# Optimization experiments

Measured on AMD Instinct MI355X. Metric: run time of the kernel, lower is better.

## Reference

```python
import jax, jax.numpy as jnp
import numpy as np

N, E, F_IN, HID, HEADS, B, CLASSES = 50000, 800000, 128, 64, 4, 512, 2


def setup_inputs() -> dict:
    key = jax.random.key(0)
    ks = jax.random.split(key, 20)
    s = 0.05
    inp = {
        "x": jax.random.normal(ks[0], (N, F_IN), jnp.float32),
        "edge_index": jax.random.randint(ks[1], (2, E), 0, N, jnp.int32),
        "batch": jnp.sort(jax.random.randint(ks[2], (N,), 0, B, jnp.int32)),
        # GCN layers (3): layer0 F_IN->HID, layers 1,2 HID->HID
        "gcn_w0": jax.random.normal(ks[3], (F_IN, HID), jnp.float32) * s,
        "gcn_b0": jnp.zeros((HID,), jnp.float32),
        "gcn_w1": jax.random.normal(ks[4], (HID, HID), jnp.float32) * s,
        "gcn_b1": jnp.zeros((HID,), jnp.float32),
        "gcn_w2": jax.random.normal(ks[5], (HID, HID), jnp.float32) * s,
        "gcn_b2": jnp.zeros((HID,), jnp.float32),
        # GAT: W [HID, HEADS*HID], attention vectors [HEADS, HID], bias [HID] (concat=False)
        "gat_w": jax.random.normal(ks[6], (HID, HEADS * HID), jnp.float32) * s,
        "gat_att_src": jax.random.normal(ks[7], (HEADS, HID), jnp.float32) * s,
        "gat_att_dst": jax.random.normal(ks[8], (HEADS, HID), jnp.float32) * s,
        "gat_b": jnp.zeros((HID,), jnp.float32),
        # MLP head
        "lin1_w": jax.random.normal(ks[9], (HID, HID // 2), jnp.float32) * s,
        "lin1_b": jnp.zeros((HID // 2,), jnp.float32),
        "lin2_w": jax.random.normal(ks[10], (HID // 2, CLASSES), jnp.float32) * s,
        "lin2_b": jnp.zeros((CLASSES,), jnp.float32),
    }
    return inp


def _forward(x, edge_index, batch,
             gcn_w0, gcn_b0, gcn_w1, gcn_b1, gcn_w2, gcn_b2,
             gat_w, gat_att_src, gat_att_dst, gat_b,
             lin1_w, lin1_b, lin2_w, lin2_b):
    n = x.shape[0]
    loop = jnp.arange(n, dtype=edge_index.dtype)
    src = jnp.concatenate([edge_index[0], loop])  # [E+N] with self-loops
    dst = jnp.concatenate([edge_index[1], loop])

    # symmetric GCN normalization (self-loops included, deg >= 1)
    deg = jax.ops.segment_sum(jnp.ones_like(dst, dtype=x.dtype), dst, num_segments=n)
    dinv = jax.lax.rsqrt(jnp.maximum(deg, 1.0))
    norm = dinv[src] * dinv[dst]  # [E+N]

    for W, b in ((gcn_w0, gcn_b0), (gcn_w1, gcn_b1), (gcn_w2, gcn_b2)):
        h = x @ W  # [N, HID]
        x = jax.ops.segment_sum(h[src] * norm[:, None], dst, num_segments=n) + b
        x = jax.nn.relu(x)  # dropout is identity in eval mode

    # GAT layer (heads=HEADS, concat=False -> mean over heads)
    H, C = gat_att_src.shape
    h = (x @ gat_w).reshape(n, H, C)  # [N, H, C]
    a_src = jnp.einsum('nhc,hc->nh', h, gat_att_src)
    a_dst = jnp.einsum('nhc,hc->nh', h, gat_att_dst)
    e = jax.nn.leaky_relu(a_src[src] + a_dst[dst], 0.2)  # [E+N, H]
    m = jax.ops.segment_max(e, dst, num_segments=n)      # per-dst softmax max
    p = jnp.exp(e - m[dst])
    denom = jax.ops.segment_sum(p, dst, num_segments=n)
    alpha = p / denom[dst]                                # [E+N, H]
    out = jax.ops.segment_sum(h[src] * alpha[:, :, None], dst, num_segments=n)
    x = jax.nn.relu(out.mean(axis=1) + gat_b)             # [N, HID]

    # global mean pool + global max pool over graphs
    cnt = jax.ops.segment_sum(jnp.ones((n,), x.dtype), batch, num_segments=B)
    mean_p = jax.ops.segment_sum(x, batch, num_segments=B) / jnp.maximum(cnt, 1.0)[:, None]
    max_p = jax.ops.segment_max(x, batch, num_segments=B)
    max_p = jnp.where(cnt[:, None] > 0, max_p, 0.0)
    g = mean_p + max_p  # [B, HID]

    g = jax.nn.relu(g @ lin1_w + lin1_b)
    return g @ lin2_w + lin2_b  # [B, CLASSES]


def reference(x, edge_index, batch,
              gcn_w0, gcn_b0, gcn_w1, gcn_b1, gcn_w2, gcn_b2,
              gat_w, gat_att_src, gat_att_dst, gat_b,
              lin1_w, lin1_b, lin2_w, lin2_b):
    return _forward(x, edge_index, batch,
                    gcn_w0, gcn_b0, gcn_w1, gcn_b1, gcn_w2, gcn_b2,
                    gat_w, gat_att_src, gat_att_dst, gat_b,
                    lin1_w, lin1_b, lin2_w, lin2_b)
```

## Files before the change

kernel.cpp:

```cpp
#include <hip/hip_runtime.h>
#include <math.h>

typedef short bf8 __attribute__((ext_vector_type(8)));
typedef _Float16 h8 __attribute__((ext_vector_type(8)));
typedef float f4 __attribute__((ext_vector_type(4)));
typedef unsigned short ushort_t;

#define BRANGE 128
#define NB_E 256

__device__ __forceinline__ int ilanebcast(int v, int l) {
  return __builtin_amdgcn_readlane(v, l);
}

__device__ __forceinline__ float wave_sum(float v) {
#pragma unroll
  for (int off = 32; off > 0; off >>= 1) v += __shfl_xor(v, off, 64);
  return v;
}

__device__ __forceinline__ ushort_t f2bf(float x) {
  unsigned int u = __float_as_uint(x);
  return (ushort_t)((u + 0x7fffu + ((u >> 16) & 1u)) >> 16);
}
__device__ __forceinline__ float b2f(ushort_t h) {
  return __uint_as_float(((unsigned int)h) << 16);
}

__global__ __launch_bounds__(256) void k_ehist(const int* __restrict__ dst,
                                               int* __restrict__ bhistT, int E, int nbuk) {
  __shared__ int h[512];
  int b = blockIdx.x, tid = threadIdx.x;
  for (int i = tid; i < nbuk; i += 256) h[i] = 0;
  __syncthreads();
  int chunk = (E + gridDim.x - 1) / gridDim.x;
  int e0 = b * chunk, e1 = min(E, e0 + chunk);
  for (int e = e0 + tid; e < e1; e += 256) atomicAdd(&h[dst[e] >> 7], 1);
  __syncthreads();
  for (int i = tid; i < nbuk; i += 256) bhistT[i * NB_E + b] = h[i];
}

__global__ __launch_bounds__(256) void k_btot(const int* __restrict__ bhistT,
                                              int* __restrict__ bcnt, int nb) {
  __shared__ int sm[256];
  int b = blockIdx.x, tid = threadIdx.x;
  sm[tid] = (tid < nb) ? bhistT[b * NB_E + tid] : 0;
  __syncthreads();
  for (int off = 128; off > 0; off >>= 1) {
    if (tid < off) sm[tid] += sm[tid + off];
    __syncthreads();
  }
  if (tid == 0) bcnt[b] = sm[0];
}

__global__ __launch_bounds__(512) void k_bscan(
    const int* __restrict__ bcnt, int* __restrict__ edgebase, int nbuk,
    int* __restrict__ rowstart, int n, int E) {
  __shared__ int smem[512];
  int t = threadIdx.x;
  int v = (t < nbuk) ? bcnt[t] : 0;
  smem[t] = v;
  __syncthreads();
  for (int off = 1; off < 512; off <<= 1) {
    int u = (t >= off) ? smem[t - off] : 0;
    __syncthreads();
    smem[t] += u;
    __syncthreads();
  }
  if (t < nbuk) edgebase[t] = smem[t] - v;
  if (t == 0) rowstart[n] = E + n;
}

__global__ __launch_bounds__(256) void k_bbase(int* __restrict__ bhistT,
                                               const int* __restrict__ edgebase,
                                               int nb) {
  __shared__ int sm[256];
  int b = blockIdx.x, tid = threadIdx.x;
  int v = (tid < nb) ? bhistT[b * NB_E + tid] : 0;
  sm[tid] = v;
  __syncthreads();
  for (int off = 1; off < 256; off <<= 1) {
    int u = (tid >= off) ? sm[tid - off] : 0;
    __syncthreads();
    sm[tid] += u;
    __syncthreads();
  }
  if (tid < nb) bhistT[b * NB_E + tid] = edgebase[b] + sm[tid] - v;
}

__global__ __launch_bounds__(256) void k_ebucket(
    const int* __restrict__ es, const int* __restrict__ ed,
    const int* __restrict__ bhistT, int* __restrict__ bedges, int E, int nbuk) {
  __shared__ int cur[512];
  int b = blockIdx.x, tid = threadIdx.x;
  for (int i = tid; i < nbuk; i += 256) cur[i] = bhistT[i * NB_E + b];
  __syncthreads();
  int chunk = (E + gridDim.x - 1) / gridDim.x;
  int e0 = b * chunk, e1 = min(E, e0 + chunk);
  for (int e = e0 + tid; e < e1; e += 256) {
    int s = es[e], d = ed[e];
    int pos = atomicAdd(&cur[d >> 7], 1);
    bedges[pos] = (s << 7) | (d & 127);
  }
}

__global__ __launch_bounds__(256) void k_ebsort(
    const int* __restrict__ bedges, const int* __restrict__ edgebase,
    const int* __restrict__ bcnt, int* __restrict__ colidx,
    int* __restrict__ rowstart, float* __restrict__ dinv, int n) {
  __shared__ int h[128];
  __shared__ int c[128];
  int b = blockIdx.x, tid = threadIdx.x;
  int nodes0 = b * BRANGE;
  int nnode = min(BRANGE, n - nodes0);
  int ebase = edgebase[b], ecnt = bcnt[b];
  int colbase = ebase + nodes0;
  if (tid < 128) h[tid] = (tid < nnode) ? 1 : 0;
  __syncthreads();
  for (int k = ebase + tid; k < ebase + ecnt; k += 256)
    atomicAdd(&h[bedges[k] & 127], 1);
  __syncthreads();
  int own = (tid < 128) ? h[tid] : 0;
  for (int off = 1; off < 128; off <<= 1) {
    int t = (tid >= off && tid < 128) ? h[tid - off] : 0;
    __syncthreads();
    if (tid < 128) h[tid] += t;
    __syncthreads();
  }
  if (tid < nnode) {
    int excl = h[tid] - own;
    int node = nodes0 + tid;
    rowstart[node] = colbase + excl;
    dinv[node] = 1.0f / sqrtf((float)own);
    colidx[colbase + excl] = node;
    c[tid] = excl + 1;
  }
  __syncthreads();
  for (int k = ebase + tid; k < ebase + ecnt; k += 256) {
    int p = bedges[k];
    int pos = atomicAdd(&c[p & 127], 1);
    colidx[colbase + pos] = p >> 7;
  }
}


__global__ void k_wswz0(const float* __restrict__ W, ushort_t* __restrict__ Bh,
                        ushort_t* __restrict__ Bl) {
  int e = blockIdx.x * 256 + threadIdx.x;
  if (e >= 4 * 4 * 64) return;
  int lane = e & 63, kc = (e >> 6) & 3, ct = e >> 8;
  int k0 = kc * 32 + (lane >> 4) * 8;
  int col = ct * 16 + (lane & 15);
#pragma unroll
  for (int j = 0; j < 8; j++) {
    float w = W[(k0 + j) * 64 + col];
    ushort_t h = f2bf(w);
    Bh[(size_t)e * 8 + j] = h;
    Bl[(size_t)e * 8 + j] = f2bf(w - b2f(h));
  }
}

__global__ void k_wswz1(const float* __restrict__ W, _Float16* __restrict__ Bh,
                        _Float16* __restrict__ Bl) {
  int e = blockIdx.x * 256 + threadIdx.x;
  if (e >= 8 * 64) return;
  int lane = e & 63, kc = (e >> 6) & 1, ct = e >> 7;
  int k0 = kc * 32 + (lane >> 4) * 8;
  int col = ct * 16 + (lane & 15);
#pragma unroll
  for (int j = 0; j < 8; j++) {
    float w = W[(k0 + j) * 64 + col];
    _Float16 h = (_Float16)w;
    Bh[(size_t)e * 8 + j] = h;
    Bl[(size_t)e * 8 + j] = (_Float16)(w - (float)h);
  }
}

__global__ void k_wswzg(const float* __restrict__ W, _Float16* __restrict__ Bh,
                        _Float16* __restrict__ Bl) {
  int e = blockIdx.x * 256 + threadIdx.x;
  if (e >= 4 * 8 * 64) return;
  int lane = e & 63, kc = (e >> 6) & 7, ct = e >> 9;
  int k0 = kc * 32 + (lane >> 4) * 8;
  int col = ct * 16 + (lane & 15);
#pragma unroll
  for (int j = 0; j < 8; j++) {
    int k = k0 + j;
    float w = W[(k & 63) * 256 + (k >> 6) * 64 + col];
    _Float16 h = (_Float16)w;
    Bh[(size_t)e * 8 + j] = h;
    Bl[(size_t)e * 8 + j] = (_Float16)(w - (float)h);
  }
}

__global__ void k_qpre(const float* __restrict__ W, const float* __restrict__ att_s,
                       const float* __restrict__ att_d,
                       float* __restrict__ q_src, float* __restrict__ q_dst) {
  int t = threadIdx.x;
  int h = t >> 6, k = t & 63;
  float ss = 0.0f, sd = 0.0f;
  for (int c = 0; c < 64; c++) {
    float w = W[k * 256 + h * 64 + c];
    ss = fmaf(w, att_s[h * 64 + c], ss);
    sd = fmaf(w, att_d[h * 64 + c], sd);
  }
  q_src[h * 64 + k] = ss;
  q_dst[h * 64 + k] = sd;
}

__global__ void k_qswz(const float* __restrict__ q_src, const float* __restrict__ q_dst,
                       _Float16* __restrict__ Bq) {
  int e = threadIdx.x;
  if (e >= 128) return;
  int lane = e & 63, kc = e >> 6;
  int k0 = kc * 32 + (lane >> 4) * 8;
  int col = lane & 15;
#pragma unroll
  for (int j = 0; j < 8; j++) {
    int k = k0 + j;
    float v = (col < 4) ? q_src[col * 64 + k]
                        : ((col < 8) ? q_dst[(col - 4) * 64 + k] : 0.0f);
    Bq[(size_t)e * 8 + j] = (_Float16)v;
  }
}

__global__ __launch_bounds__(256) void k_gemm0_mfma(
    const float* __restrict__ X, const ushort_t* __restrict__ Bh,
    const ushort_t* __restrict__ Bl, const float* __restrict__ dinv,
    _Float16* __restrict__ H, int n, int ntiles) {
  int tid = threadIdx.x, lane = tid & 63, wave = tid >> 6;
  int m = lane & 15, q = lane >> 4;
  for (int tile = blockIdx.x * 4 + wave; tile < ntiles; tile += gridDim.x * 4) {
    int ra = tile * 16 + m;
    if (ra >= n) ra = n - 1;
    const float* xrow = X + (size_t)ra * 128;
    f4 acc[4];
#pragma unroll
    for (int ct = 0; ct < 4; ct++) acc[ct] = (f4){0.f, 0.f, 0.f, 0.f};
#pragma unroll 2
    for (int kc = 0; kc < 4; kc++) {
      int ko = kc * 32 + q * 8;
      float4 xa = *(const float4*)(xrow + ko);
      float4 xb = *(const float4*)(xrow + ko + 4);
      float f[8] = {xa.x, xa.y, xa.z, xa.w, xb.x, xb.y, xb.z, xb.w};
      union { ushort_t u[8]; bf8 v; } Uh, Ul;
#pragma unroll
      for (int j = 0; j < 8; j++) {
        ushort_t h = f2bf(f[j]);
        Uh.u[j] = h;
        Ul.u[j] = f2bf(f[j] - b2f(h));
      }
#pragma unroll
      for (int ct = 0; ct < 4; ct++) {
        size_t boff = ((size_t)(ct * 4 + kc) * 64 + lane) * 8;
        bf8 bh = *(const bf8*)(Bh + boff);
        bf8 bl = *(const bf8*)(Bl + boff);
        acc[ct] = __builtin_amdgcn_mfma_f32_16x16x32_bf16(Uh.v, bh, acc[ct], 0, 0, 0);
        acc[ct] = __builtin_amdgcn_mfma_f32_16x16x32_bf16(Ul.v, bh, acc[ct], 0, 0, 0);
        acc[ct] = __builtin_amdgcn_mfma_f32_16x16x32_bf16(Uh.v, bl, acc[ct], 0, 0, 0);
      }
    }
#pragma unroll
    for (int r = 0; r < 4; r++) {
      int row = tile * 16 + q * 4 + r;
      if (row < n) {
        float dv = dinv[row];
#pragma unroll
        for (int ct = 0; ct < 4; ct++)
          H[(size_t)row * 64 + ct * 16 + m] = (_Float16)(acc[ct][r] * dv);
      }
    }
  }
}

__device__ __forceinline__ float gather_sum(const _Float16* __restrict__ h_in,
                                            const int* __restrict__ colidx,
                                            int s0, int s1, int lane) {
  float acc = 0.0f, accB = 0.0f;
  for (int base = s0; base < s1; base += 64) {
    int cnt = min(64, s1 - base);
    int myidx = (lane < cnt) ? colidx[base + lane] : 0;
    int k = 0;
    for (; k + 3 < cnt; k += 4) {
      int sa = ilanebcast(myidx, k);
      int sb = ilanebcast(myidx, k + 1);
      int sc = ilanebcast(myidx, k + 2);
      int sd = ilanebcast(myidx, k + 3);
      float va = (float)h_in[((size_t)sa << 6) + lane];
      float vb = (float)h_in[((size_t)sb << 6) + lane];
      float vc = (float)h_in[((size_t)sc << 6) + lane];
      float vd = (float)h_in[((size_t)sd << 6) + lane];
      acc += va; accB += vb; acc += vc; accB += vd;
    }
    for (; k < cnt; k++) {
      int sa = ilanebcast(myidx, k);
      acc += (float)h_in[((size_t)sa << 6) + lane];
    }
  }
  return acc + accB;
}

__global__ __launch_bounds__(1024) void k_agg_gemm_mfma(
    const _Float16* __restrict__ h_in, const float* __restrict__ dinv,
    const int* __restrict__ rowstart, const int* __restrict__ colidx,
    const float* __restrict__ bias, const _Float16* __restrict__ Bh,
    const _Float16* __restrict__ Bl, _Float16* __restrict__ h_out, int n) {
  __shared__ __align__(16) _Float16 xstage[16][72];
  int tid = threadIdx.x, lane = tid & 63, w = tid >> 6;
  int tile = blockIdx.x;
  int node = tile * 16 + w;
  float xv = 0.0f;
  if (node < n) {
    int s0 = rowstart[node], s1 = rowstart[node + 1];
    float a = gather_sum(h_in, colidx, s0, s1, lane);
    xv = fmaxf(fmaf(dinv[node], a, bias[lane]), 0.0f);
  }
  xstage[w][lane] = (_Float16)xv;
  __syncthreads();
  if (w < 4) {
    int m = lane & 15, q = lane >> 4, ct = w;
    h8 af0 = *(const h8*)&xstage[m][q * 8];
    h8 af1 = *(const h8*)&xstage[m][32 + q * 8];
    size_t o0 = ((size_t)(ct * 2 + 0) * 64 + lane) * 8;
    size_t o1 = ((size_t)(ct * 2 + 1) * 64 + lane) * 8;
    h8 bh0 = *(const h8*)(Bh + o0);
    h8 bh1 = *(const h8*)(Bh + o1);
    h8 bl0 = *(const h8*)(Bl + o0);
    h8 bl1 = *(const h8*)(Bl + o1);
    f4 acc = (f4){0.f, 0.f, 0.f, 0.f};
    acc = __builtin_amdgcn_mfma_f32_16x16x32_f16(af0, bh0, acc, 0, 0, 0);
    acc = __builtin_amdgcn_mfma_f32_16x16x32_f16(af1, bh1, acc, 0, 0, 0);
    acc = __builtin_amdgcn_mfma_f32_16x16x32_f16(af0, bl0, acc, 0, 0, 0);
    acc = __builtin_amdgcn_mfma_f32_16x16x32_f16(af1, bl1, acc, 0, 0, 0);
#pragma unroll
    for (int r = 0; r < 4; r++) {
      int n2 = tile * 16 + q * 4 + r;
      if (n2 < n)
        h_out[(size_t)n2 * 64 + ct * 16 + m] = (_Float16)(acc[r] * dinv[n2]);
    }
  }
}

__global__ __launch_bounds__(1024) void k_agg_gatpre_mfma(
    const _Float16* __restrict__ h_in, const float* __restrict__ dinv,
    const int* __restrict__ rowstart, const int* __restrict__ colidx,
    const float* __restrict__ bias, const _Float16* __restrict__ Bq,
    _Float16* __restrict__ x3, float* __restrict__ a_src, float* __restrict__ a_dst,
    int n) {
  __shared__ __align__(16) _Float16 xstage[16][72];
  int tid = threadIdx.x, lane = tid & 63, w = tid >> 6;
  int tile = blockIdx.x;
  int node = tile * 16 + w;
  float xv = 0.0f;
  if (node < n) {
    int s0 = rowstart[node], s1 = rowstart[node + 1];
    float a = gather_sum(h_in, colidx, s0, s1, lane);
    xv = fmaxf(fmaf(dinv[node], a, bias[lane]), 0.0f);
    x3[((size_t)node << 6) + lane] = (_Float16)xv;
  }
  xstage[w][lane] = (_Float16)xv;
  __syncthreads();
  if (w == 0) {
    int m = lane & 15, q = lane >> 4;
    h8 af0 = *(const h8*)&xstage[m][q * 8];
    h8 af1 = *(const h8*)&xstage[m][32 + q * 8];
    h8 bq0 = *(const h8*)(Bq + (size_t)lane * 8);
    h8 bq1 = *(const h8*)(Bq + (size_t)(64 + lane) * 8);
    f4 accL = (f4){0.f, 0.f, 0.f, 0.f};
    accL = __builtin_amdgcn_mfma_f32_16x16x32_f16(af0, bq0, accL, 0, 0, 0);
    accL = __builtin_amdgcn_mfma_f32_16x16x32_f16(af1, bq1, accL, 0, 0, 0);
#pragma unroll
    for (int r = 0; r < 4; r++) {
      int n2 = tile * 16 + q * 4 + r;
      if (n2 < n) {
        if (m < 4) a_src[(size_t)n2 * 4 + m] = accL[r];
        else if (m < 8) a_dst[(size_t)n2 * 4 + (m - 4)] = accL[r];
      }
    }
  }
}

__global__ __launch_bounds__(1024) void k_gat_fused(
    const _Float16* __restrict__ x3, const float* __restrict__ a_src,
    const float* __restrict__ a_dst, const int* __restrict__ rowstart,
    const int* __restrict__ colidx, const _Float16* __restrict__ Bh,
    const _Float16* __restrict__ Bl, const float* __restrict__ bias,
    float* __restrict__ out, int n) {
  __shared__ __align__(16) float4 wlds[16][64];
  __shared__ __align__(16) float astage[16][260];
  int tid = threadIdx.x, lane = tid & 63, w = tid >> 6;
  int tile = blockIdx.x;
  int node = tile * 16 + w;
  float v0 = 0.f, v1 = 0.f, v2 = 0.f, v3 = 0.f;
  if (node < n) {
    const float4 adv = *(const float4*)&a_dst[(size_t)node * 4];
    int s0 = rowstart[node], s1 = rowstart[node + 1];
    float acc0 = 0, acc1 = 0, acc2 = 0, acc3 = 0;
    float S0 = 0, S1 = 0, S2 = 0, S3 = 0;
    for (int base = s0; base < s1; base += 64) {
      int cnt = min(64, s1 - base);
      bool act = (lane < cnt);
      int myidx = act ? colidx[base + lane] : 0;
      float w0 = 0, w1 = 0, w2 = 0, w3 = 0;
      if (act) {
        const float4 as = *(const float4*)&a_src[(size_t)myidx * 4];
        float e0 = as.x + adv.x; e0 = (e0 > 0.f) ? e0 : 0.2f * e0; w0 = __expf(e0);
        float e1 = as.y + adv.y; e1 = (e1 > 0.f) ? e1 : 0.2f * e1; w1 = __expf(e1);
        float e2 = as.z + adv.z; e2 = (e2 > 0.f) ? e2 : 0.2f * e2; w2 = __expf(e2);
        float e3 = as.w + adv.w; e3 = (e3 > 0.f) ? e3 : 0.2f * e3; w3 = __expf(e3);
      }
      S0 += wave_sum(w0); S1 += wave_sum(w1);
      S2 += wave_sum(w2); S3 += wave_sum(w3);
      wlds[w][lane] = make_float4(w0, w1, w2, w3);
      int k = 0;
      for (; k + 3 < cnt; k += 4) {
        int sa = ilanebcast(myidx, k);
        int sb = ilanebcast(myidx, k + 1);
        int sc = ilanebcast(myidx, k + 2);
        int sd = ilanebcast(myidx, k + 3);
        float4 wa = wlds[w][k];
        float4 wb = wlds[w][k + 1];
        float4 wc = wlds[w][k + 2];
        float4 wd = wlds[w][k + 3];
        float va = (float)x3[((size_t)sa << 6) + lane];
        float vb = (float)x3[((size_t)sb << 6) + lane];
        float vc = (float)x3[((size_t)sc << 6) + lane];
        float vd = (float)x3[((size_t)sd << 6) + lane];
        acc0 = fmaf(wa.x, va, acc0); acc1 = fmaf(wa.y, va, acc1);
        acc2 = fmaf(wa.z, va, acc2); acc3 = fmaf(wa.w, va, acc3);
        acc0 = fmaf(wb.x, vb, acc0); acc1 = fmaf(wb.y, vb, acc1);
        acc2 = fmaf(wb.z, vb, acc2); acc3 = fmaf(wb.w, vb, acc3);
        acc0 = fmaf(wc.x, vc, acc0); acc1 = fmaf(wc.y, vc, acc1);
        acc2 = fmaf(wc.z, vc, acc2); acc3 = fmaf(wc.w, vc, acc3);
        acc0 = fmaf(wd.x, vd, acc0); acc1 = fmaf(wd.y, vd, acc1);
        acc2 = fmaf(wd.z, vd, acc2); acc3 = fmaf(wd.w, vd, acc3);
      }
      for (; k < cnt; k++) {
        int sa = ilanebcast(myidx, k);
        float4 wa = wlds[w][k];
        float va = (float)x3[((size_t)sa << 6) + lane];
        acc0 = fmaf(wa.x, va, acc0); acc1 = fmaf(wa.y, va, acc1);
        acc2 = fmaf(wa.z, va, acc2); acc3 = fmaf(wa.w, va, acc3);
      }
    }
    v0 = acc0 * (0.25f / S0);
    v1 = acc1 * (0.25f / S1);
    v2 = acc2 * (0.25f / S2);
    v3 = acc3 * (0.25f / S3);
  }
  astage[w][lane] = v0;
  astage[w][64 + lane] = v1;
  astage[w][128 + lane] = v2;
  astage[w][192 + lane] = v3;
  __syncthreads();
  if (w < 4) {
    int m = lane & 15, q = lane >> 4, ct = w;
    float bv = bias[ct * 16 + m];
    f4 acc = (f4){0.f, 0.f, 0.f, 0.f};
#pragma unroll 2
    for (int kc = 0; kc < 8; kc++) {
      const float* ap = &astage[m][kc * 32 + q * 8];
      union { _Float16 u[8]; h8 v; } Uh, Ul;
#pragma unroll
      for (int j = 0; j < 8; j++) {
        float a = ap[j];
        _Float16 h = (_Float16)a;
        Uh.u[j] = h;
        Ul.u[j] = (_Float16)(a - (float)h);
      }
      size_t boff = ((size_t)(ct * 8 + kc) * 64 + lane) * 8;
      h8 bh = *(const h8*)(Bh + boff);
      h8 bl = *(const h8*)(Bl + boff);
      acc = __builtin_amdgcn_mfma_f32_16x16x32_f16(Uh.v, bh, acc, 0, 0, 0);
      acc = __builtin_amdgcn_mfma_f32_16x16x32_f16(Ul.v, bh, acc, 0, 0, 0);
      acc = __builtin_amdgcn_mfma_f32_16x16x32_f16(Uh.v, bl, acc, 0, 0, 0);
    }
#pragma unroll
    for (int r = 0; r < 4; r++) {
      int row = tile * 16 + q * 4 + r;
      if (row < n)
        out[(size_t)row * 64 + ct * 16 + m] = fmaxf(acc[r] + bv, 0.f);
    }
  }
}

__global__ void k_gstart(const int* __restrict__ batch, int* gs, int n, int B) {
  int g = blockIdx.x * blockDim.x + threadIdx.x;
  if (g > B) return;
  int lo = 0, hi = n;
  while (lo < hi) {
    int mid = (lo + hi) >> 1;
    if (batch[mid] < g) lo = mid + 1; else hi = mid;
  }
  gs[g] = lo;
}

__global__ __launch_bounds__(256) void k_pool(const float* __restrict__ x,
                                              const int* __restrict__ gs,
                                              float* __restrict__ gvec, int B) {
  int g = (blockIdx.x * blockDim.x + threadIdx.x) >> 6;
  int lane = threadIdx.x & 63;
  if (g >= B) return;
  int s0 = gs[g], s1 = gs[g + 1];
  float sum = 0.0f, mx = -INFINITY;
  for (int nd = s0; nd < s1; ++nd) {
    float v = x[(size_t)nd * 64 + lane];
    sum += v;
    mx = fmaxf(mx, v);
  }
  int cnt = s1 - s0;
  float mean = sum / fmaxf((float)cnt, 1.0f);
  float mp = (cnt > 0) ? mx : 0.0f;
  gvec[g * 64 + lane] = mean + mp;
}

__global__ __launch_bounds__(256) void k_mlp(const float* __restrict__ gvec,
                                             const float* __restrict__ w1,
                                             const float* __restrict__ b1,
                                             const float* __restrict__ w2,
                                             const float* __restrict__ b2,
                                             float* __restrict__ out, int B) {
  int g = blockIdx.x * blockDim.x + threadIdx.x;
  if (g >= B) return;
  float gv[64];
#pragma unroll
  for (int i = 0; i < 64; i++) gv[i] = gvec[g * 64 + i];
  float o0 = b2[0], o1 = b2[1];
  for (int j = 0; j < 32; j++) {
    float a = b1[j];
#pragma unroll
    for (int i = 0; i < 64; i++) a = fmaf(gv[i], w1[i * 32 + j], a);
    a = fmaxf(a, 0.0f);
    o0 = fmaf(a, w2[j * 2 + 0], o0);
    o1 = fmaf(a, w2[j * 2 + 1], o1);
  }
  out[g * 2 + 0] = o0;
  out[g * 2 + 1] = o1;
}

extern "C" void kernel_launch(void* const* d_in, const int* in_sizes, int n_in,
                              void* d_out, int out_size, void* d_ws, size_t ws_size,
                              hipStream_t stream) {
  const float* x     = (const float*)d_in[0];
  const int*   ei    = (const int*)d_in[1];
  const int*   batch = (const int*)d_in[2];
  const float* w0 = (const float*)d_in[3];  const float* b0 = (const float*)d_in[4];
  const float* w1 = (const float*)d_in[5];  const float* b1 = (const float*)d_in[6];
  const float* w2 = (const float*)d_in[7];  const float* b2 = (const float*)d_in[8];
  const float* gat_w = (const float*)d_in[9];
  const float* att_s = (const float*)d_in[10];
  const float* att_d = (const float*)d_in[11];
  const float* gat_b = (const float*)d_in[12];
  const float* l1w = (const float*)d_in[13]; const float* l1b = (const float*)d_in[14];
  const float* l2w = (const float*)d_in[15]; const float* l2b = (const float*)d_in[16];

  const int N = in_sizes[0] / 128;
  const int E = in_sizes[1] / 2;
  const int B = out_size / 2;
  const int NT = (N + 15) / 16;
  const int NBUK = (N + BRANGE - 1) / BRANGE;

  char* ws = (char*)d_ws;
  size_t off = 0;
  auto alloc = [&](size_t bytes) -> void* {
    void* p = ws + off;
    off = (off + bytes + 255) & ~(size_t)255;
    return p;
  };
  int*       bhistT   = (int*)alloc((size_t)NBUK * NB_E * 4);
  int*       edgebase = (int*)alloc((size_t)NBUK * 4);
  int*       bcnt     = (int*)alloc((size_t)NBUK * 4);
  int*       bedges   = (int*)alloc((size_t)E * 4);
  int*       rowstart = (int*)alloc((size_t)(N + 1) * 4);
  int*       colidx   = (int*)alloc((size_t)(E + N) * 4);
  float*     dinv     = (float*)alloc((size_t)N * 4);
  _Float16*  hbuf     = (_Float16*)alloc((size_t)N * 64 * 2);
  _Float16*  hbuf2    = (_Float16*)alloc((size_t)N * 64 * 2);
  _Float16*  xg       = (_Float16*)alloc((size_t)N * 64 * 2);
  float*     gatout   = (float*)alloc((size_t)N * 64 * 4);
  float*     a_src    = (float*)alloc((size_t)N * 4 * 4);
  float*     a_dst    = (float*)alloc((size_t)N * 4 * 4);
  float*     q_src    = (float*)alloc(4 * 64 * 4);
  float*     q_dst    = (float*)alloc(4 * 64 * 4);
  ushort_t*  B0h      = (ushort_t*)alloc(4 * 4 * 64 * 8 * 2);
  ushort_t*  B0l      = (ushort_t*)alloc(4 * 4 * 64 * 8 * 2);
  _Float16*  Bw1h     = (_Float16*)alloc(8 * 64 * 8 * 2);
  _Float16*  Bw1l     = (_Float16*)alloc(8 * 64 * 8 * 2);
  _Float16*  Bw2h     = (_Float16*)alloc(8 * 64 * 8 * 2);
  _Float16*  Bw2l     = (_Float16*)alloc(8 * 64 * 8 * 2);
  _Float16*  Bq       = (_Float16*)alloc(2 * 64 * 8 * 2);
  _Float16*  Bgh      = (_Float16*)alloc(4 * 8 * 64 * 8 * 2);
  _Float16*  Bgl      = (_Float16*)alloc(4 * 8 * 64 * 8 * 2);
  int*       gs       = (int*)alloc((size_t)(B + 1) * 4);
  float*     gvec     = (float*)alloc((size_t)B * 64 * 4);
  (void)ws_size; (void)n_in;

  k_ehist<<<NB_E, 256, 0, stream>>>(ei + E, bhistT, E, NBUK);
  k_btot<<<NBUK, 256, 0, stream>>>(bhistT, bcnt, NB_E);
  k_bscan<<<1, 512, 0, stream>>>(bcnt, edgebase, NBUK, rowstart, N, E);
  k_bbase<<<NBUK, 256, 0, stream>>>(bhistT, edgebase, NB_E);
  k_ebucket<<<NB_E, 256, 0, stream>>>(ei, ei + E, bhistT, bedges, E, NBUK);
  k_ebsort<<<NBUK, 256, 0, stream>>>(bedges, edgebase, bcnt, colidx, rowstart, dinv, N);
  k_qpre<<<1, 256, 0, stream>>>(gat_w, att_s, att_d, q_src, q_dst);
  k_qswz<<<1, 256, 0, stream>>>(q_src, q_dst, Bq);
  k_wswz0<<<4, 256, 0, stream>>>(w0, B0h, B0l);
  k_wswz1<<<2, 256, 0, stream>>>(w1, Bw1h, Bw1l);
  k_wswz1<<<2, 256, 0, stream>>>(w2, Bw2h, Bw2l);
  k_wswzg<<<8, 256, 0, stream>>>(gat_w, Bgh, Bgl);

  k_gemm0_mfma<<<1024, 256, 0, stream>>>(x, B0h, B0l, dinv, hbuf, N, NT);
  k_agg_gemm_mfma<<<NT, 1024, 0, stream>>>(hbuf, dinv, rowstart, colidx, b0,
                                           Bw1h, Bw1l, hbuf2, N);
  k_agg_gemm_mfma<<<NT, 1024, 0, stream>>>(hbuf2, dinv, rowstart, colidx, b1,
                                           Bw2h, Bw2l, hbuf, N);
  k_agg_gatpre_mfma<<<NT, 1024, 0, stream>>>(hbuf, dinv, rowstart, colidx, b2,
                                             Bq, xg, a_src, a_dst, N);
  k_gat_fused<<<NT, 1024, 0, stream>>>(xg, a_src, a_dst, rowstart, colidx,
                                       Bgh, Bgl, gat_b, gatout, N);
  k_gstart<<<(B + 1 + 255) / 256, 256, 0, stream>>>(batch, gs, N, B);
  k_pool<<<(B + 3) / 4, 256, 0, stream>>>(gatout, gs, gvec, B);
  k_mlp<<<(B + 255) / 256, 256, 0, stream>>>(gvec, l1w, l1b, l2w, l2b, (float*)d_out, B);
}
```

Before: 373.4 us.

## Balance edge work across waves within each 16-node tile using LDS atomics

The two GCN aggregation kernels and the fused GAT kernel now split a tile's whole edge range evenly across its 16 waves, instead of giving each wave one node's edges. Each wave walks the node segments its slice covers and combines partial sums into shared memory with atomic adds; the GAT kernel also accumulates its softmax denominators there and normalizes afterwards. The aim is to remove imbalance caused by nodes with very different degrees within a tile. In exchange it adds LDS zeroing, extra barriers, atomics and per-segment setup overhead.

```diff
diff --git a/kernel.cpp b/kernel.cpp
--- a/kernel.cpp
+++ b/kernel.cpp
@@ -273,9 +273,9 @@
   }
 }
 
-__device__ __forceinline__ float gather_sum(const _Float16* __restrict__ h_in,
-                                            const int* __restrict__ colidx,
-                                            int s0, int s1, int lane) {
+__device__ __forceinline__ float gather_range(const _Float16* __restrict__ h_in,
+                                              const int* __restrict__ colidx,
+                                              int s0, int s1, int lane) {
   float acc = 0.0f, accB = 0.0f;
   for (int base = s0; base < s1; base += 64) {
     int cnt = min(64, s1 - base);
@@ -305,16 +305,38 @@
     const int* __restrict__ rowstart, const int* __restrict__ colidx,
     const float* __restrict__ bias, const _Float16* __restrict__ Bh,
     const _Float16* __restrict__ Bl, _Float16* __restrict__ h_out, int n) {
+  __shared__ float fstage[16][64];
   __shared__ __align__(16) _Float16 xstage[16][72];
+  __shared__ int rs[17];
   int tid = threadIdx.x, lane = tid & 63, w = tid >> 6;
   int tile = blockIdx.x;
+  if (tid < 17) rs[tid] = rowstart[min(tile * 16 + tid, n)];
+  fstage[w][lane] = 0.0f;
+  __syncthreads();
+  int e0 = rs[0], e1 = rs[16];
+  int per = (e1 - e0 + 15) >> 4;
+  int my0 = e0 + w * per;
+  int my1 = min(e1, my0 + per);
+  if (my0 < my1) {
+    int seg = 0;
+    while (rs[seg + 1] <= my0) seg++;
+    int e = my0;
+    while (e < my1) {
+      int send = min(my1, rs[seg + 1]);
+      if (send > e) {
+        float acc = gather_range(h_in, colidx, e, send, lane);
+        atomicAdd(&fstage[seg][lane], acc);
+      }
+      seg++;
+      e = (send > e) ? send : e;
+      if (seg >= 16) break;
+    }
+  }
+  __syncthreads();
   int node = tile * 16 + w;
   float xv = 0.0f;
-  if (node < n) {
-    int s0 = rowstart[node], s1 = rowstart[node + 1];
-    float a = gather_sum(h_in, colidx, s0, s1, lane);
-    xv = fmaxf(fmaf(dinv[node], a, bias[lane]), 0.0f);
-  }
+  if (node < n)
+    xv = fmaxf(fmaf(dinv[node], fstage[w][lane], bias[lane]), 0.0f);
   xstage[w][lane] = (_Float16)xv;
   __syncthreads();
   if (w < 4) {
@@ -347,15 +369,38 @@
     const float* __restrict__ bias, const _Float16* __restrict__ Bq,
     _Float16* __restrict__ x3, float* __restrict__ a_src, float* __restrict__ a_dst,
     int n) {
+  __shared__ float fstage[16][64];
   __shared__ __align__(16) _Float16 xstage[16][72];
+  __shared__ int rs[17];
   int tid = threadIdx.x, lane = tid & 63, w = tid >> 6;
   int tile = blockIdx.x;
+  if (tid < 17) rs[tid] = rowstart[min(tile * 16 + tid, n)];
+  fstage[w][lane] = 0.0f;
+  __syncthreads();
+  int e0 = rs[0], e1 = rs[16];
+  int per = (e1 - e0 + 15) >> 4;
+  int my0 = e0 + w * per;
+  int my1 = min(e1, my0 + per);
+  if (my0 < my1) {
+    int seg = 0;
+    while (rs[seg + 1] <= my0) seg++;
+    int e = my0;
+    while (e < my1) {
+      int send = min(my1, rs[seg + 1]);
+      if (send > e) {
+        float acc = gather_range(h_in, colidx, e, send, lane);
+        atomicAdd(&fstage[seg][lane], acc);
+      }
+      seg++;
+      e = (send > e) ? send : e;
+      if (seg >= 16) break;
+    }
+  }
+  __syncthreads();
   int node = tile * 16 + w;
   float xv = 0.0f;
   if (node < n) {
-    int s0 = rowstart[node], s1 = rowstart[node + 1];
-    float a = gather_sum(h_in, colidx, s0, s1, lane);
-    xv = fmaxf(fmaf(dinv[node], a, bias[lane]), 0.0f);
+    xv = fmaxf(fmaf(dinv[node], fstage[w][lane], bias[lane]), 0.0f);
     x3[((size_t)node << 6) + lane] = (_Float16)xv;
   }
   xstage[w][lane] = (_Float16)xv;
@@ -387,71 +432,95 @@
     const _Float16* __restrict__ Bl, const float* __restrict__ bias,
     float* __restrict__ out, int n) {
   __shared__ __align__(16) float4 wlds[16][64];
-  __shared__ __align__(16) float astage[16][260];
+  __shared__ float astage[16][261];
+  __shared__ float Sstage[16][4];
+  __shared__ int rs[17];
   int tid = threadIdx.x, lane = tid & 63, w = tid >> 6;
   int tile = blockIdx.x;
-  int node = tile * 16 + w;
-  float v0 = 0.f, v1 = 0.f, v2 = 0.f, v3 = 0.f;
-  if (node < n) {
-    const float4 adv = *(const float4*)&a_dst[(size_t)node * 4];
-    int s0 = rowstart[node], s1 = rowstart[node + 1];
-    float acc0 = 0, acc1 = 0, acc2 = 0, acc3 = 0;
-    float S0 = 0, S1 = 0, S2 = 0, S3 = 0;
-    for (int base = s0; base < s1; base += 64) {
-      int cnt = min(64, s1 - base);
-      bool act = (lane < cnt);
-      int myidx = act ? colidx[base + lane] : 0;
-      float w0 = 0, w1 = 0, w2 = 0, w3 = 0;
-      if (act) {
-        const float4 as = *(const float4*)&a_src[(size_t)myidx * 4];
-        float e0 = as.x + adv.x; e0 = (e0 > 0.f) ? e0 : 0.2f * e0; w0 = __expf(e0);
-        float e1 = as.y + adv.y; e1 = (e1 > 0.f) ? e1 : 0.2f * e1; w1 = __expf(e1);
-        float e2 = as.z + adv.z; e2 = (e2 > 0.f) ? e2 : 0.2f * e2; w2 = __expf(e2);
-        float e3 = as.w + adv.w; e3 = (e3 > 0.f) ? e3 : 0.2f * e3; w3 = __expf(e3);
-      }
-      S0 += wave_sum(w0); S1 += wave_sum(w1);
-      S2 += wave_sum(w2); S3 += wave_sum(w3);
-      wlds[w][lane] = make_float4(w0, w1, w2, w3);
-      int k = 0;
-      for (; k + 3 < cnt; k += 4) {
-        int sa = ilanebcast(myidx, k);
-        int sb = ilanebcast(myidx, k + 1);
-        int sc = ilanebcast(myidx, k + 2);
-        int sd = ilanebcast(myidx, k + 3);
-        float4 wa = wlds[w][k];
-        float4 wb = wlds[w][k + 1];
-        float4 wc = wlds[w][k + 2];
-        float4 wd = wlds[w][k + 3];
-        float va = (float)x3[((size_t)sa << 6) + lane];
-        float vb = (float)x3[((size_t)sb << 6) + lane];
-        float vc = (float)x3[((size_t)sc << 6) + lane];
-        float vd = (float)x3[((size_t)sd << 6) + lane];
-        acc0 = fmaf(wa.x, va, acc0); acc1 = fmaf(wa.y, va, acc1);
-        acc2 = fmaf(wa.z, va, acc2); acc3 = fmaf(wa.w, va, acc3);
-        acc0 = fmaf(wb.x, vb, acc0); acc1 = fmaf(wb.y, vb, acc1);
-        acc2 = fmaf(wb.z, vb, acc2); acc3 = fmaf(wb.w, vb, acc3);
-        acc0 = fmaf(wc.x, vc, acc0); acc1 = fmaf(wc.y, vc, acc1);
-        acc2 = fmaf(wc.z, vc, acc2); acc3 = fmaf(wc.w, vc, acc3);
-        acc0 = fmaf(wd.x, vd, acc0); acc1 = fmaf(wd.y, vd, acc1);
-        acc2 = fmaf(wd.z, vd, acc2); acc3 = fmaf(wd.w, vd, acc3);
-      }
-      for (; k < cnt; k++) {
-        int sa = ilanebcast(myidx, k);
-        float4 wa = wlds[w][k];
-        float va = (float)x3[((size_t)sa << 6) + lane];
-        acc0 = fmaf(wa.x, va, acc0); acc1 = fmaf(wa.y, va, acc1);
-        acc2 = fmaf(wa.z, va, acc2); acc3 = fmaf(wa.w, va, acc3);
-      }
-    }
-    v0 = acc0 * (0.25f / S0);
-    v1 = acc1 * (0.25f / S1);
-    v2 = acc2 * (0.25f / S2);
-    v3 = acc3 * (0.25f / S3);
-  }
-  astage[w][lane] = v0;
-  astage[w][64 + lane] = v1;
-  astage[w][128 + lane] = v2;
-  astage[w][192 + lane] = v3;
+  if (tid < 17) rs[tid] = rowstart[min(tile * 16 + tid, n)];
+  for (int i = tid; i < 16 * 261; i += 1024) ((float*)astage)[i] = 0.0f;
+  if (tid < 64) ((float*)Sstage)[tid] = 0.0f;
+  __syncthreads();
+  int e0 = rs[0], e1 = rs[16];
+  int per = (e1 - e0 + 15) >> 4;
+  int my0 = e0 + w * per;
+  int my1 = min(e1, my0 + per);
+  if (my0 < my1) {
+    int seg = 0;
+    while (rs[seg + 1] <= my0) seg++;
+    int e = my0;
+    while (e < my1) {
+      int send = min(my1, rs[seg + 1]);
+      if (send > e) {
+        int node_s = tile * 16 + seg;
+        const float4 adv = *(const float4*)&a_dst[(size_t)node_s * 4];
+        float acc0 = 0, acc1 = 0, acc2 = 0, acc3 = 0;
+        float S0 = 0, S1 = 0, S2 = 0, S3 = 0;
+        for (int base = e; base < send; base += 64) {
+          int cnt = min(64, send - base);
+          bool act = (lane < cnt);
+          int myidx = act ? colidx[base + lane] : 0;
+          float w0 = 0, w1 = 0, w2 = 0, w3 = 0;
+          if (act) {
+            const float4 as = *(const float4*)&a_src[(size_t)myidx * 4];
+            float q0 = as.x + adv.x; q0 = (q0 > 0.f) ? q0 : 0.2f * q0; w0 = __expf(q0);
+            float q1 = as.y + adv.y; q1 = (q1 > 0.f) ? q1 : 0.2f * q1; w1 = __expf(q1);
+            float q2 = as.z + adv.z; q2 = (q2 > 0.f) ? q2 : 0.2f * q2; w2 = __expf(q2);
+            float q3 = as.w + adv.w; q3 = (q3 > 0.f) ? q3 : 0.2f * q3; w3 = __expf(q3);
+          }
+          S0 += wave_sum(w0); S1 += wave_sum(w1);
+          S2 += wave_sum(w2); S3 += wave_sum(w3);
+          wlds[w][lane] = make_float4(w0, w1, w2, w3);
+          int k = 0;
+          for (; k + 3 < cnt; k += 4) {
+            int sa = ilanebcast(myidx, k);
+            int sb = ilanebcast(myidx, k + 1);
+            int sc = ilanebcast(myidx, k + 2);
+            int sd = ilanebcast(myidx, k + 3);
+            float4 wa = wlds[w][k];
+            float4 wb = wlds[w][k + 1];
+            float4 wc = wlds[w][k + 2];
+            float4 wd = wlds[w][k + 3];
+            float va = (float)x3[((size_t)sa << 6) + lane];
+            float vb = (float)x3[((size_t)sb << 6) + lane];
+            float vc = (float)x3[((size_t)sc << 6) + lane];
+            float vd = (float)x3[((size_t)sd << 6) + lane];
+            acc0 = fmaf(wa.x, va, acc0); acc1 = fmaf(wa.y, va, acc1);
+            acc2 = fmaf(wa.z, va, acc2); acc3 = fmaf(wa.w, va, acc3);
+            acc0 = fmaf(wb.x, vb, acc0); acc1 = fmaf(wb.y, vb, acc1);
+            acc2 = fmaf(wb.z, vb, acc2); acc3 = fmaf(wb.w, vb, acc3);
+            acc0 = fmaf(wc.x, vc, acc0); acc1 = fmaf(wc.y, vc, acc1);
+            acc2 = fmaf(wc.z, vc, acc2); acc3 = fmaf(wc.w, vc, acc3);
+            acc0 = fmaf(wd.x, vd, acc0); acc1 = fmaf(wd.y, vd, acc1);
+            acc2 = fmaf(wd.z, vd, acc2); acc3 = fmaf(wd.w, vd, acc3);
+          }
+          for (; k < cnt; k++) {
+            int sa = ilanebcast(myidx, k);
+            float4 wa = wlds[w][k];
+            float va = (float)x3[((size_t)sa << 6) + lane];
+            acc0 = fmaf(wa.x, va, acc0); acc1 = fmaf(wa.y, va, acc1);
+            acc2 = fmaf(wa.z, va, acc2); acc3 = fmaf(wa.w, va, acc3);
+          }
+        }
+        atomicAdd(&astage[seg][lane], acc0);
+        atomicAdd(&astage[seg][64 + lane], acc1);
+        atomicAdd(&astage[seg][128 + lane], acc2);
+        atomicAdd(&astage[seg][192 + lane], acc3);
+        float sv = (lane == 0) ? S0 : (lane == 1) ? S1 : (lane == 2) ? S2 : S3;
+        if (lane < 4) atomicAdd(&Sstage[seg][lane], sv);
+      }
+      seg++;
+      e = (send > e) ? send : e;
+      if (seg >= 16) break;
+    }
+  }
+  __syncthreads();
+  if (tile * 16 + w < n) {
+    astage[w][lane]       *= 0.25f / Sstage[w][0];
+    astage[w][64 + lane]  *= 0.25f / Sstage[w][1];
+    astage[w][128 + lane] *= 0.25f / Sstage[w][2];
+    astage[w][192 + lane] *= 0.25f / Sstage[w][3];
+  }
   __syncthreads();
   if (w < 4) {
     int m = lane & 15, q = lane >> 4, ct = w;
```

Measured after the change: 583.5 us. 56.3% more time.
